# Kernel optimization log

Hardware: AMD Instinct MI355X
Metric: run time of the kernel (lower is better)

The kernel has to match this reference:

```python
import jax, jax.numpy as jnp
import numpy as np

CTX = 2048
N_EMBD = 1024
HEAD = 128

def setup_inputs() -> dict:
    key = jax.random.key(0)
    kx, kq, kk, kv = jax.random.split(key, 4)
    s = 1.0 / np.sqrt(N_EMBD)
    return {
        "x": jax.random.normal(kx, (4, CTX, N_EMBD), dtype=jnp.float32),
        "Wq": jax.random.normal(kq, (N_EMBD, HEAD), dtype=jnp.float32) * s,
        "Wk": jax.random.normal(kk, (N_EMBD, HEAD), dtype=jnp.float32) * s,
        "Wv": jax.random.normal(kv, (N_EMBD, HEAD), dtype=jnp.float32) * s,
    }

def reference(x, Wq, Wk, Wv):
    B, T, C = x.shape
    q = jnp.einsum('btc,ch->bth', x, Wq)
    k = jnp.einsum('btc,ch->bth', x, Wk)
    v = jnp.einsum('btc,ch->bth', x, Wv)
    scale = 1.0 / jnp.sqrt(jnp.asarray(k.shape[-1], dtype=x.dtype))
    wei = jnp.einsum('bth,bsh->bts', q, k) * scale  # [B,T,T]
    causal = jnp.tril(jnp.ones((T, T), dtype=bool))
    wei = jnp.where(causal, wei, jnp.asarray(-jnp.inf, dtype=wei.dtype))
    wei = jax.nn.softmax(wei, axis=-1)
    out = jnp.einsum('bts,bsh->bth', wei, v)
    return out
```

## Files before the change

kernel.cpp:

```cpp
#include <hip/hip_runtime.h>

#define BATCH 4
#define CTX   2048
#define EMB   1024
#define HEAD  128

typedef __attribute__((ext_vector_type(8))) short bf16x8;
typedef __attribute__((ext_vector_type(4))) float f32x4;
typedef const __attribute__((address_space(1))) unsigned int* gas_t;
typedef __attribute__((address_space(3))) unsigned int* las_t;

#define FINF (__builtin_inff())
__device__ inline float fexp2(float x) { return __builtin_amdgcn_exp2f(x); }

__device__ inline void cp16(const void* g, void* l) {
    __builtin_amdgcn_global_load_lds((gas_t)g, (las_t)l, 16, 0, 0);
}

__device__ inline unsigned short f2bf(float f) {
    union { float f; unsigned u; } v; v.f = f;
    unsigned r = v.u + 0x7fffu + ((v.u >> 16) & 1u);
    return (unsigned short)(r >> 16);
}
__device__ inline unsigned pk2(float a, float b) {
    return (unsigned)f2bf(a) | ((unsigned)f2bf(b) << 16);
}
__device__ inline float bf2f(unsigned u16) {
    union { unsigned u; float f; } v; v.u = u16 << 16; return v.f;
}

__global__ __launch_bounds__(256)
void transpose_w_kernel(const float* __restrict__ Wq, const float* __restrict__ Wk,
                        const float* __restrict__ Wv, unsigned short* __restrict__ Wt) {
    const int k0 = blockIdx.x * 64;
    const int h0 = blockIdx.y * 64;
    const int w  = blockIdx.z;
    const float* W = (w == 0) ? Wq : (w == 1) ? Wk : Wv;
    __shared__ float Ts[64][65];
    const int tid = threadIdx.x;
    #pragma unroll
    for (int it = 0; it < 4; ++it) {
        const int kk = (tid >> 4) + it * 16;
        const int c4 = (tid & 15) * 4;
        const float4 f = *(const float4*)&W[(size_t)(k0 + kk) * HEAD + h0 + c4];
        Ts[kk][c4 + 0] = f.x; Ts[kk][c4 + 1] = f.y;
        Ts[kk][c4 + 2] = f.z; Ts[kk][c4 + 3] = f.w;
    }
    __syncthreads();
    const int hr  = tid >> 2;
    const int kc0 = (tid & 3) * 16;
    union { unsigned short s[16]; uint4 q[2]; } tmp;
    #pragma unroll
    for (int i = 0; i < 16; ++i) tmp.s[i] = f2bf(Ts[kc0 + i][hr]);
    unsigned short* dst = &Wt[(size_t)w * HEAD * EMB + (size_t)(h0 + hr) * EMB + k0 + kc0];
    ((uint4*)dst)[0] = tmp.q[0];
    ((uint4*)dst)[1] = tmp.q[1];
}

__global__ __launch_bounds__(128, 3)
void proj_kernel(const float* __restrict__ x, const unsigned short* __restrict__ Wt,
                 unsigned short* __restrict__ qb, unsigned short* __restrict__ kb,
                 unsigned short* __restrict__ vt) {
    __shared__ __align__(16) char smem[24576];
    char* Ab = smem;
    char* Bb = smem + 8192;

    const int wsel = blockIdx.y;
    const int tid  = threadIdx.x;
    const int wv   = tid >> 6;
    const int lane = tid & 63;
    const int p = lane >> 4, c = lane & 15;
    const int m0 = blockIdx.x * 32;
    const unsigned short* Wp = Wt + (size_t)wsel * HEAD * EMB;

    const int u7  = c & 7;
    const int u2c = (c ^ (c >> 2)) & 3;

    auto stage = [&](int bi, int ks) {
        #pragma unroll
        for (int i = 0; i < 2; ++i) {
            const int f = i * 128 + tid;
            const int r = f >> 3, s = f & 7, q = s ^ (r & 7);
            cp16(&x[(size_t)(m0 + r) * EMB + ks * 32 + q * 4],
                 Ab + bi * 4096 + i * 2048 + wv * 1024);
        }
        #pragma unroll
        for (int i = 0; i < 4; ++i) {
            const int f = i * 128 + tid;
            const int h = f >> 2, s = f & 3, q = s ^ ((h ^ (h >> 2)) & 3);
            cp16(&Wp[(size_t)h * EMB + ks * 32 + q * 8],
                 Bb + bi * 8192 + i * 2048 + wv * 1024);
        }
    };
    auto xfrag = [&](const char* Ac, int r) {
        const float4 a0 = *(const float4*)(Ac + r * 128 + (((2 * p)     ^ u7) * 16));
        const float4 a1 = *(const float4*)(Ac + r * 128 + (((2 * p + 1) ^ u7) * 16));
        union { unsigned u[4]; bf16x8 v; } xf;
        xf.u[0] = pk2(a0.x, a0.y); xf.u[1] = pk2(a0.z, a0.w);
        xf.u[2] = pk2(a1.x, a1.y); xf.u[3] = pk2(a1.z, a1.w);
        return xf.v;
    };

    if (wsel < 2) {
        f32x4 acc[8];
        #pragma unroll
        for (int i = 0; i < 8; ++i) acc[i] = (f32x4){0.f, 0.f, 0.f, 0.f};
        stage(0, 0);
        for (int ks = 0; ks < 32; ++ks) {
            const int cur = ks & 1;
            __syncthreads();
            if (ks + 1 < 32) stage(cur ^ 1, ks + 1);
            const bf16x8 xv = xfrag(Ab + cur * 4096, wv * 16 + c);
            const char* Bc = Bb + cur * 8192;
            #pragma unroll
            for (int nt = 0; nt < 8; ++nt) {
                const int h = nt * 16 + c;
                const bf16x8 wf = *(const bf16x8*)(Bc + h * 64 + ((p ^ u2c) * 16));
                acc[nt] = __builtin_amdgcn_mfma_f32_16x16x32_bf16(xv, wf, acc[nt], 0, 0, 0);
            }
        }
        unsigned short* outp = (wsel == 0) ? qb : kb;
        #pragma unroll
        for (int rr = 0; rr < 4; ++rr) {
            unsigned short* orow = outp + (size_t)(m0 + wv * 16 + p * 4 + rr) * HEAD + c;
            #pragma unroll
            for (int nt = 0; nt < 8; ++nt)
                orow[nt * 16] = f2bf(acc[nt][rr]);
        }
    } else {
        f32x4 acc[4][2];
        #pragma unroll
        for (int i = 0; i < 4; ++i)
            #pragma unroll
            for (int j = 0; j < 2; ++j) acc[i][j] = (f32x4){0.f, 0.f, 0.f, 0.f};
        stage(0, 0);
        for (int ks = 0; ks < 32; ++ks) {
            const int cur = ks & 1;
            __syncthreads();
            if (ks + 1 < 32) stage(cur ^ 1, ks + 1);
            const char* Ac = Ab + cur * 4096;
            const char* Bc = Bb + cur * 8192;
            bf16x8 xv[2];
            #pragma unroll
            for (int n2 = 0; n2 < 2; ++n2) xv[n2] = xfrag(Ac, n2 * 16 + c);
            #pragma unroll
            for (int mt = 0; mt < 4; ++mt) {
                const int h = wv * 64 + mt * 16 + c;
                const bf16x8 wf = *(const bf16x8*)(Bc + h * 64 + ((p ^ u2c) * 16));
                #pragma unroll
                for (int n2 = 0; n2 < 2; ++n2)
                    acc[mt][n2] = __builtin_amdgcn_mfma_f32_16x16x32_bf16(wf, xv[n2], acc[mt][n2], 0, 0, 0);
            }
        }
        const int bidx = m0 >> 11;
        const int tl   = m0 & (CTX - 1);
        unsigned short* vbp = vt + (size_t)bidx * HEAD * CTX;
        #pragma unroll
        for (int mt = 0; mt < 4; ++mt)
            #pragma unroll
            for (int rr = 0; rr < 4; ++rr) {
                const int h = wv * 64 + mt * 16 + p * 4 + rr;
                #pragma unroll
                for (int n2 = 0; n2 < 2; ++n2)
                    vbp[(size_t)h * CTX + tl + n2 * 16 + c] = f2bf(acc[mt][n2][rr]);
            }
    }
}

__global__ __launch_bounds__(256, 2)
void attn_split_kernel(const unsigned short* __restrict__ qb,
                       const unsigned short* __restrict__ kb,
                       const unsigned short* __restrict__ vt,
                       unsigned short* __restrict__ pO,
                       float* __restrict__ pM, float* __restrict__ pL) {
    __shared__ __align__(16) char smem[65536];
    char* Kb = smem;
    char* Vb = smem + 32768;

    const int g = blockIdx.x;
    const int b = blockIdx.y;
    int T, ch;
    if (g < 8)       { T = g;                ch = 0; }
    else if (g < 24) { T = 8  + ((g - 8) >> 1);  ch = (g - 8) & 1; }
    else if (g < 48) { T = 16 + (g - 24) / 3;    ch = (g - 24) % 3; }
    else             { T = 24 + ((g - 48) >> 2); ch = (g - 48) & 3; }
    const int nch    = (T >> 3) + 1;
    const int kstart = ch * 512;
    const int kend   = min(kstart + 512, 64 * (T + 1));
    const int nsteps = (kend - kstart) >> 6;
    const bool lastchunk = (ch == nch - 1);

    const int tid  = threadIdx.x;
    const int wv   = tid >> 6;
    const int lane = tid & 63;
    const int p = lane >> 4, c = lane & 15;
    const int t0 = T * 64;
    const int qg = t0 + wv * 16 + c;
    const int u7 = c & 7;

    const unsigned short* kbat = kb + (size_t)b * CTX * HEAD;
    const unsigned short* vbat = vt + (size_t)b * HEAD * CTX;

    bf16x8 qf[4];
    #pragma unroll
    for (int ks = 0; ks < 4; ++ks)
        qf[ks] = *(const bf16x8*)&qb[((size_t)b * CTX + t0 + wv * 16 + c) * HEAD + ks * 32 + p * 8];

    f32x4 o[8];
    #pragma unroll
    for (int i = 0; i < 8; ++i) o[i] = (f32x4){0.f, 0.f, 0.f, 0.f};
    float m = -FINF, l = 0.f;

    const int  slA = 32 * (p & 1) + c;
    const int  slB = slA + 16;
    const bool thi = (p >> 1) != 0;
    const float scale2 = 0.08838834764831845f * 1.44269504088896340f;

    auto stage = [&](int bi, int js) {
        const unsigned short* kg = kbat + (size_t)(kstart + js * 64) * HEAD;
        #pragma unroll
        for (int i = 0; i < 4; ++i) {
            const int f = i * 256 + tid;
            const int r = f >> 4, s = f & 15, q = s ^ (r & 7);
            cp16(kg + (size_t)r * HEAD + q * 8, Kb + bi * 16384 + (f >> 6) * 1024);
        }
        const unsigned short* vg = vbat + kstart + js * 64;
        #pragma unroll
        for (int i = 0; i < 4; ++i) {
            const int f = i * 256 + tid;
            const int r = f >> 3, s = f & 7, q = s ^ (r & 7);
            cp16(vg + (size_t)r * CTX + q * 8, Vb + bi * 16384 + (f >> 6) * 1024);
        }
    };

    stage(0, 0);
    for (int js = 0; js < nsteps; ++js) {
        const int cur = js & 1;
        __builtin_amdgcn_s_waitcnt(0);
        __syncthreads();

        bf16x8 kfr[4][4];
        #pragma unroll
        for (int nt = 0; nt < 4; ++nt) {
            const char* rp = Kb + cur * 16384 + (nt * 16 + c) * 256;
            #pragma unroll
            for (int ks = 0; ks < 4; ++ks)
                kfr[nt][ks] = *(const bf16x8*)(rp + (((ks * 4 + p) ^ u7) * 16));
        }
        if (js + 1 < nsteps) stage(cur ^ 1, js + 1);

        f32x4 st[4];
        #pragma unroll
        for (int nt = 0; nt < 4; ++nt) st[nt] = (f32x4){0.f, 0.f, 0.f, 0.f};
        #pragma unroll
        for (int ks = 0; ks < 4; ++ks)
            #pragma unroll
            for (int nt = 0; nt < 4; ++nt)
                st[nt] = __builtin_amdgcn_mfma_f32_16x16x32_bf16(kfr[nt][ks], qf[ks], st[nt], 0, 0, 0);

        bf16x8 vfr[2][8];
        #pragma unroll
        for (int mt = 0; mt < 8; ++mt) {
            const char* rp = Vb + cur * 16384 + (mt * 16 + c) * 128;
            #pragma unroll
            for (int ch2 = 0; ch2 < 2; ++ch2)
                vfr[ch2][mt] = *(const bf16x8*)(rp + (((ch2 * 4 + p) ^ u7) * 16));
        }

        float s[4][4];
        float lm = -FINF;
        if (lastchunk && js == nsteps - 1) {
            #pragma unroll
            for (int nt = 0; nt < 4; ++nt)
                #pragma unroll
                for (int r = 0; r < 4; ++r) {
                    const int kv = kstart + js * 64 + nt * 16 + p * 4 + r;
                    float v = st[nt][r] * scale2;
                    v = (kv <= qg) ? v : -FINF;
                    s[nt][r] = v;
                    lm = fmaxf(lm, v);
                }
        } else {
            #pragma unroll
            for (int nt = 0; nt < 4; ++nt)
                #pragma unroll
                for (int r = 0; r < 4; ++r) {
                    const float v = st[nt][r] * scale2;
                    s[nt][r] = v;
                    lm = fmaxf(lm, v);
                }
        }
        lm = fmaxf(lm, __shfl_xor(lm, 16, 64));
        lm = fmaxf(lm, __shfl_xor(lm, 32, 64));
        const float m_new = fmaxf(m, lm);
        const float alpha = fexp2(m - m_new);
        float ls = 0.f;
        #pragma unroll
        for (int nt = 0; nt < 4; ++nt)
            #pragma unroll
            for (int r = 0; r < 4; ++r) {
                const float pv = fexp2(s[nt][r] - m_new);
                s[nt][r] = pv;
                ls += pv;
            }
        ls += __shfl_xor(ls, 16, 64);
        ls += __shfl_xor(ls, 32, 64);
        l = l * alpha + ls;
        m = m_new;
        #pragma unroll
        for (int i = 0; i < 8; ++i) {
            o[i][0] *= alpha; o[i][1] *= alpha;
            o[i][2] *= alpha; o[i][3] *= alpha;
        }
        #pragma unroll
        for (int ch2 = 0; ch2 < 2; ++ch2) {
            const unsigned pa0 = pk2(s[2*ch2][0],     s[2*ch2][1]);
            const unsigned pb0 = pk2(s[2*ch2][2],     s[2*ch2][3]);
            const unsigned pa1 = pk2(s[2*ch2 + 1][0], s[2*ch2 + 1][1]);
            const unsigned pb1 = pk2(s[2*ch2 + 1][2], s[2*ch2 + 1][3]);
            const unsigned u0a = __shfl((int)pa0, slA, 64), u0b = __shfl((int)pa1, slA, 64);
            const unsigned u1a = __shfl((int)pb0, slA, 64), u1b = __shfl((int)pb1, slA, 64);
            const unsigned u2a = __shfl((int)pa0, slB, 64), u2b = __shfl((int)pa1, slB, 64);
            const unsigned u3a = __shfl((int)pb0, slB, 64), u3b = __shfl((int)pb1, slB, 64);
            union { unsigned u[4]; bf16x8 v; } pf;
            pf.u[0] = thi ? u0b : u0a;
            pf.u[1] = thi ? u1b : u1a;
            pf.u[2] = thi ? u2b : u2a;
            pf.u[3] = thi ? u3b : u3a;
            #pragma unroll
            for (int mt = 0; mt < 8; ++mt)
                o[mt] = __builtin_amdgcn_mfma_f32_16x16x32_bf16(vfr[ch2][mt], pf.v, o[mt], 0, 0, 0);
        }
    }

    const size_t pbase = (size_t)(b * 32 + T) * 4 + ch;
    unsigned short* po = pO + pbase * (64 * 128) + (wv * 16 + c) * 128;
    #pragma unroll
    for (int mt = 0; mt < 8; ++mt) {
        union { unsigned short sh[4]; uint2 u; } t;
        #pragma unroll
        for (int r = 0; r < 4; ++r) t.sh[r] = f2bf(o[mt][r]);
        *(uint2*)&po[mt * 16 + p * 4] = t.u;
    }
    if (p == 0) {
        pM[pbase * 64 + wv * 16 + c] = m;
        pL[pbase * 64 + wv * 16 + c] = l;
    }
}

__global__ __launch_bounds__(256)
void attn_merge_kernel(const unsigned short* __restrict__ pO,
                       const float* __restrict__ pM, const float* __restrict__ pL,
                       float* __restrict__ out) {
    const int T = blockIdx.x, b = blockIdx.y;
    const int nch = (T >> 3) + 1;
    const int tid = threadIdx.x;
    const int r   = tid >> 2;
    const int c0  = (tid & 3) * 32;
    const size_t base = (size_t)(b * 32 + T) * 4;

    float mv[4], lv[4];
    float M = -FINF;
    #pragma unroll
    for (int i = 0; i < 4; ++i) {
        if (i < nch) { mv[i] = pM[(base + i) * 64 + r]; lv[i] = pL[(base + i) * 64 + r]; }
        else         { mv[i] = -FINF;                   lv[i] = 0.f; }
        M = fmaxf(M, mv[i]);
    }
    float w[4], L = 0.f;
    #pragma unroll
    for (int i = 0; i < 4; ++i) { w[i] = fexp2(mv[i] - M); L += w[i] * lv[i]; }
    const float inv = 1.f / L;

    float acc[32];
    #pragma unroll
    for (int j = 0; j < 32; ++j) acc[j] = 0.f;
    #pragma unroll
    for (int i = 0; i < 4; ++i) {
        if (i < nch) {
            const unsigned* s32 = (const unsigned*)(pO + (base + i) * (64 * 128) + r * 128 + c0);
            const float wi = w[i];
            #pragma unroll
            for (int jw = 0; jw < 16; ++jw) {
                const unsigned u = s32[jw];
                acc[2 * jw]     += wi * bf2f(u & 0xffffu);
                acc[2 * jw + 1] += wi * bf2f(u >> 16);
            }
        }
    }
    float* orow = out + ((size_t)b * CTX + T * 64 + r) * HEAD + c0;
    #pragma unroll
    for (int j4 = 0; j4 < 8; ++j4) {
        float4 ov = make_float4(acc[4*j4] * inv, acc[4*j4+1] * inv,
                                acc[4*j4+2] * inv, acc[4*j4+3] * inv);
        *(float4*)&orow[4 * j4] = ov;
    }
}

__global__ __launch_bounds__(64, 1)
void attn_kernel(const unsigned short* __restrict__ qb,
                 const unsigned short* __restrict__ kb,
                 const unsigned short* __restrict__ vt,
                 float* __restrict__ out) {
    __shared__ __align__(16) char smem[65536];
    char* Kb = smem;
    char* Vb = smem + 32768;
    const int bx   = blockIdx.x;
    const int b    = bx & 3;
    const int tile = 127 - (bx >> 2);
    const int lane = threadIdx.x;
    const int p = lane >> 4, c = lane & 15;
    const int t0 = tile * 16;
    const int qg = t0 + c;
    const int u7 = c & 7;
    const unsigned short* kbat = kb + (size_t)b * CTX * HEAD;
    const unsigned short* vbat = vt + (size_t)b * HEAD * CTX;
    bf16x8 qf[4];
    #pragma unroll
    for (int ks = 0; ks < 4; ++ks)
        qf[ks] = *(const bf16x8*)&qb[((size_t)b * CTX + t0 + c) * HEAD + ks * 32 + p * 8];
    f32x4 o[8];
    #pragma unroll
    for (int i = 0; i < 8; ++i) o[i] = (f32x4){0.f, 0.f, 0.f, 0.f};
    float m = -FINF, l = 0.f;
    const int  slA = 32 * (p & 1) + c;
    const int  slB = slA + 16;
    const bool thi = (p >> 1) != 0;
    const int  nsteps = (tile + 4) >> 2;
    const float scale2 = 0.08838834764831845f * 1.44269504088896340f;
    auto stage = [&](int bi, int js) {
        const unsigned short* kg = kbat + (size_t)(js * 64) * HEAD;
        #pragma unroll
        for (int i = 0; i < 16; ++i) {
            const int f = i * 64 + lane;
            const int r = f >> 4, s = f & 15, q = s ^ (r & 7);
            cp16(kg + (size_t)r * HEAD + q * 8, Kb + bi * 16384 + i * 1024);
        }
        #pragma unroll
        for (int i = 0; i < 16; ++i) {
            const int f = i * 64 + lane;
            const int r = f >> 3, s = f & 7, q = s ^ (r & 7);
            cp16(vbat + (size_t)r * CTX + js * 64 + q * 8, Vb + bi * 16384 + i * 1024);
        }
    };
    stage(0, 0);
    for (int js = 0; js < nsteps; ++js) {
        const int cur = js & 1;
        __builtin_amdgcn_s_waitcnt(0);
        bf16x8 kfr[4][4], vfr[2][8];
        #pragma unroll
        for (int nt = 0; nt < 4; ++nt) {
            const char* rp = Kb + cur * 16384 + (nt * 16 + c) * 256;
            #pragma unroll
            for (int ks = 0; ks < 4; ++ks)
                kfr[nt][ks] = *(const bf16x8*)(rp + (((ks * 4 + p) ^ u7) * 16));
        }
        #pragma unroll
        for (int mt = 0; mt < 8; ++mt) {
            const char* rp = Vb + cur * 16384 + (mt * 16 + c) * 128;
            #pragma unroll
            for (int ch = 0; ch < 2; ++ch)
                vfr[ch][mt] = *(const bf16x8*)(rp + (((ch * 4 + p) ^ u7) * 16));
        }
        if (js + 1 < nsteps) stage(cur ^ 1, js + 1);
        const int c0 = js * 64;
        f32x4 st[4];
        #pragma unroll
        for (int nt = 0; nt < 4; ++nt) st[nt] = (f32x4){0.f, 0.f, 0.f, 0.f};
        #pragma unroll
        for (int ks = 0; ks < 4; ++ks)
            #pragma unroll
            for (int nt = 0; nt < 4; ++nt)
                st[nt] = __builtin_amdgcn_mfma_f32_16x16x32_bf16(kfr[nt][ks], qf[ks], st[nt], 0, 0, 0);
        float s[4][4];
        float lm = -FINF;
        if (js == nsteps - 1) {
            #pragma unroll
            for (int nt = 0; nt < 4; ++nt)
                #pragma unroll
                for (int r = 0; r < 4; ++r) {
                    const int kv = c0 + nt * 16 + p * 4 + r;
                    float v = st[nt][r] * scale2;
                    v = (kv <= qg) ? v : -FINF;
                    s[nt][r] = v;
                    lm = fmaxf(lm, v);
                }
        } else {
            #pragma unroll
            for (int nt = 0; nt < 4; ++nt)
                #pragma unroll
                for (int r = 0; r < 4; ++r) {
                    const float v = st[nt][r] * scale2;
                    s[nt][r] = v;
                    lm = fmaxf(lm, v);
                }
        }
        lm = fmaxf(lm, __shfl_xor(lm, 16, 64));
        lm = fmaxf(lm, __shfl_xor(lm, 32, 64));
        const float m_new = fmaxf(m, lm);
        const float alpha = fexp2(m - m_new);
        float ls = 0.f;
        #pragma unroll
        for (int nt = 0; nt < 4; ++nt)
            #pragma unroll
            for (int r = 0; r < 4; ++r) {
                const float pv = fexp2(s[nt][r] - m_new);
                s[nt][r] = pv;
                ls += pv;
            }
        ls += __shfl_xor(ls, 16, 64);
        ls += __shfl_xor(ls, 32, 64);
        l = l * alpha + ls;
        m = m_new;
        #pragma unroll
        for (int i = 0; i < 8; ++i) {
            o[i][0] *= alpha; o[i][1] *= alpha;
            o[i][2] *= alpha; o[i][3] *= alpha;
        }
        #pragma unroll
        for (int ch = 0; ch < 2; ++ch) {
            const unsigned pa0 = pk2(s[2*ch][0],     s[2*ch][1]);
            const unsigned pb0 = pk2(s[2*ch][2],     s[2*ch][3]);
            const unsigned pa1 = pk2(s[2*ch + 1][0], s[2*ch + 1][1]);
            const unsigned pb1 = pk2(s[2*ch + 1][2], s[2*ch + 1][3]);
            const unsigned u0a = __shfl((int)pa0, slA, 64), u0b = __shfl((int)pa1, slA, 64);
            const unsigned u1a = __shfl((int)pb0, slA, 64), u1b = __shfl((int)pb1, slA, 64);
            const unsigned u2a = __shfl((int)pa0, slB, 64), u2b = __shfl((int)pa1, slB, 64);
            const unsigned u3a = __shfl((int)pb0, slB, 64), u3b = __shfl((int)pb1, slB, 64);
            union { unsigned u[4]; bf16x8 v; } pf;
            pf.u[0] = thi ? u0b : u0a;
            pf.u[1] = thi ? u1b : u1a;
            pf.u[2] = thi ? u2b : u2a;
            pf.u[3] = thi ? u3b : u3a;
            #pragma unroll
            for (int mt = 0; mt < 8; ++mt)
                o[mt] = __builtin_amdgcn_mfma_f32_16x16x32_bf16(vfr[ch][mt], pf.v, o[mt], 0, 0, 0);
        }
    }
    const float linv = 1.f / l;
    float* orow = out + ((size_t)b * CTX + t0 + c) * HEAD;
    #pragma unroll
    for (int mt = 0; mt < 8; ++mt) {
        float4 ov = make_float4(o[mt][0] * linv, o[mt][1] * linv,
                                o[mt][2] * linv, o[mt][3] * linv);
        *(float4*)&orow[mt * 16 + p * 4] = ov;
    }
}

extern "C" void kernel_launch(void* const* d_in, const int* in_sizes, int n_in,
                              void* d_out, int out_size, void* d_ws, size_t ws_size,
                              hipStream_t stream) {
    const float* x  = (const float*)d_in[0];
    const float* Wq = (const float*)d_in[1];
    const float* Wk = (const float*)d_in[2];
    const float* Wv = (const float*)d_in[3];
    float* out = (float*)d_out;

    unsigned short* Wt = (unsigned short*)d_ws;
    unsigned short* qb = Wt + (size_t)3 * HEAD * EMB;
    unsigned short* kb = qb + (size_t)BATCH * CTX * HEAD;
    unsigned short* vt = kb + (size_t)BATCH * CTX * HEAD;
    unsigned short* pO = vt + (size_t)BATCH * CTX * HEAD;
    float* pM = (float*)(pO + (size_t)BATCH * 32 * 4 * 64 * 128);
    float* pL = pM + (size_t)BATCH * 32 * 4 * 64;

    const size_t need = (size_t)((char*)(pL + BATCH * 32 * 4 * 64) - (char*)d_ws);

    transpose_w_kernel<<<dim3(16, 2, 3), 256, 0, stream>>>(Wq, Wk, Wv, Wt);
    proj_kernel<<<dim3((BATCH * CTX) / 32, 3), 128, 0, stream>>>(x, Wt, qb, kb, vt);
    if (ws_size >= need) {
        attn_split_kernel<<<dim3(80, 4), 256, 0, stream>>>(qb, kb, vt, pO, pM, pL);
        attn_merge_kernel<<<dim3(32, 4), 256, 0, stream>>>(pO, pM, pL, out);
    } else {
        attn_kernel<<<BATCH * (CTX / 16), 64, 0, stream>>>(qb, kb, vt, out);
    }
}
```

Baseline: 126.0 us.

## Halve attention KV chunk size and give each wave two query subtiles

The split-KV attention kernel now uses 256-key chunks instead of 512, which raises the grid from 80 to 144 blocks per batch. Blocks shrink to 128 threads, with each wave handling two 16-row query subtiles so K/V fragments loaded from LDS are reused across both. The aim is better load balance and more parallelism across CUs for the causal workload, plus more reuse of each K/V fragment. In exchange it doubles per-wave register state, drops the occupancy hint to 1, and makes the merge kernel combine up to 8 partials with more partial-output traffic.

Result: slower. 131.5 us (+4.4%).

```diff
diff --git a/kernel.cpp b/kernel.cpp
--- a/kernel.cpp
+++ b/kernel.cpp
@@ -167,7 +167,7 @@
     }
 }
 
-__global__ __launch_bounds__(256, 2)
+__global__ __launch_bounds__(128, 1)
 void attn_split_kernel(const unsigned short* __restrict__ qb,
                        const unsigned short* __restrict__ kb,
                        const unsigned short* __restrict__ vt,
@@ -179,37 +179,41 @@
 
     const int g = blockIdx.x;
     const int b = blockIdx.y;
-    int T, ch;
-    if (g < 8)       { T = g;                ch = 0; }
-    else if (g < 24) { T = 8  + ((g - 8) >> 1);  ch = (g - 8) & 1; }
-    else if (g < 48) { T = 16 + (g - 24) / 3;    ch = (g - 24) % 3; }
-    else             { T = 24 + ((g - 48) >> 2); ch = (g - 48) & 3; }
-    const int nch    = (T >> 3) + 1;
-    const int kstart = ch * 512;
-    const int kend   = min(kstart + 512, 64 * (T + 1));
-    const int nsteps = (kend - kstart) >> 6;
-    const bool lastchunk = (ch == nch - 1);
+    int a = 0;
+    while (a < 7 && g >= 2 * (a + 1) * (a + 2)) ++a;
+    const int rem = g - 2 * a * (a + 1);
+    const int T   = 4 * a + rem / (a + 1);
+    const int ch  = rem % (a + 1);
+    const bool lastchunk = (ch == a);
+    const int kstart = ch * 256;
+    const int nsteps = lastchunk ? ((T & 3) + 1) : 4;
 
     const int tid  = threadIdx.x;
     const int wv   = tid >> 6;
     const int lane = tid & 63;
     const int p = lane >> 4, c = lane & 15;
     const int t0 = T * 64;
-    const int qg = t0 + wv * 16 + c;
     const int u7 = c & 7;
+    int qg[2];
+    qg[0] = t0 + wv * 32 + c;
+    qg[1] = qg[0] + 16;
 
     const unsigned short* kbat = kb + (size_t)b * CTX * HEAD;
     const unsigned short* vbat = vt + (size_t)b * HEAD * CTX;
 
-    bf16x8 qf[4];
-    #pragma unroll
-    for (int ks = 0; ks < 4; ++ks)
-        qf[ks] = *(const bf16x8*)&qb[((size_t)b * CTX + t0 + wv * 16 + c) * HEAD + ks * 32 + p * 8];
-
-    f32x4 o[8];
-    #pragma unroll
-    for (int i = 0; i < 8; ++i) o[i] = (f32x4){0.f, 0.f, 0.f, 0.f};
-    float m = -FINF, l = 0.f;
+    bf16x8 qf[2][4];
+    #pragma unroll
+    for (int qs = 0; qs < 2; ++qs)
+        #pragma unroll
+        for (int ks = 0; ks < 4; ++ks)
+            qf[qs][ks] = *(const bf16x8*)&qb[((size_t)b * CTX + t0 + wv * 32 + qs * 16 + c) * HEAD + ks * 32 + p * 8];
+
+    f32x4 o[2][8];
+    #pragma unroll
+    for (int qs = 0; qs < 2; ++qs)
+        #pragma unroll
+        for (int i = 0; i < 8; ++i) o[qs][i] = (f32x4){0.f, 0.f, 0.f, 0.f};
+    float m2[2] = {-FINF, -FINF}, l2[2] = {0.f, 0.f};
 
     const int  slA = 32 * (p & 1) + c;
     const int  slB = slA + 16;
@@ -219,15 +223,15 @@
     auto stage = [&](int bi, int js) {
         const unsigned short* kg = kbat + (size_t)(kstart + js * 64) * HEAD;
         #pragma unroll
-        for (int i = 0; i < 4; ++i) {
-            const int f = i * 256 + tid;
+        for (int i = 0; i < 8; ++i) {
+            const int f = i * 128 + tid;
             const int r = f >> 4, s = f & 15, q = s ^ (r & 7);
             cp16(kg + (size_t)r * HEAD + q * 8, Kb + bi * 16384 + (f >> 6) * 1024);
         }
         const unsigned short* vg = vbat + kstart + js * 64;
         #pragma unroll
-        for (int i = 0; i < 4; ++i) {
-            const int f = i * 256 + tid;
+        for (int i = 0; i < 8; ++i) {
+            const int f = i * 128 + tid;
             const int r = f >> 3, s = f & 7, q = s ^ (r & 7);
             cp16(vg + (size_t)r * CTX + q * 8, Vb + bi * 16384 + (f >> 6) * 1024);
         }
@@ -249,102 +253,114 @@
         }
         if (js + 1 < nsteps) stage(cur ^ 1, js + 1);
 
-        f32x4 st[4];
-        #pragma unroll
-        for (int nt = 0; nt < 4; ++nt) st[nt] = (f32x4){0.f, 0.f, 0.f, 0.f};
+        f32x4 st[2][4];
+        #pragma unroll
+        for (int qs = 0; qs < 2; ++qs)
+            #pragma unroll
+            for (int nt = 0; nt < 4; ++nt) st[qs][nt] = (f32x4){0.f, 0.f, 0.f, 0.f};
         #pragma unroll
         for (int ks = 0; ks < 4; ++ks)
             #pragma unroll
-            for (int nt = 0; nt < 4; ++nt)
-                st[nt] = __builtin_amdgcn_mfma_f32_16x16x32_bf16(kfr[nt][ks], qf[ks], st[nt], 0, 0, 0);
+            for (int nt = 0; nt < 4; ++nt) {
+                st[0][nt] = __builtin_amdgcn_mfma_f32_16x16x32_bf16(kfr[nt][ks], qf[0][ks], st[0][nt], 0, 0, 0);
+                st[1][nt] = __builtin_amdgcn_mfma_f32_16x16x32_bf16(kfr[nt][ks], qf[1][ks], st[1][nt], 0, 0, 0);
+            }
 
         bf16x8 vfr[2][8];
         #pragma unroll
         for (int mt = 0; mt < 8; ++mt) {
             const char* rp = Vb + cur * 16384 + (mt * 16 + c) * 128;
             #pragma unroll
-            for (int ch2 = 0; ch2 < 2; ++ch2)
-                vfr[ch2][mt] = *(const bf16x8*)(rp + (((ch2 * 4 + p) ^ u7) * 16));
-        }
-
-        float s[4][4];
-        float lm = -FINF;
-        if (lastchunk && js == nsteps - 1) {
+            for (int c2 = 0; c2 < 2; ++c2)
+                vfr[c2][mt] = *(const bf16x8*)(rp + (((c2 * 4 + p) ^ u7) * 16));
+        }
+
+        const bool domask = lastchunk && (js == nsteps - 1);
+        float s[2][4][4];
+        #pragma unroll
+        for (int qs = 0; qs < 2; ++qs) {
+            float lm = -FINF;
+            if (domask) {
+                #pragma unroll
+                for (int nt = 0; nt < 4; ++nt)
+                    #pragma unroll
+                    for (int r = 0; r < 4; ++r) {
+                        const int kv = kstart + js * 64 + nt * 16 + p * 4 + r;
+                        float v = st[qs][nt][r] * scale2;
+                        v = (kv <= qg[qs]) ? v : -FINF;
+                        s[qs][nt][r] = v;
+                        lm = fmaxf(lm, v);
+                    }
+            } else {
+                #pragma unroll
+                for (int nt = 0; nt < 4; ++nt)
+                    #pragma unroll
+                    for (int r = 0; r < 4; ++r) {
+                        const float v = st[qs][nt][r] * scale2;
+                        s[qs][nt][r] = v;
+                        lm = fmaxf(lm, v);
+                    }
+            }
+            lm = fmaxf(lm, __shfl_xor(lm, 16, 64));
+            lm = fmaxf(lm, __shfl_xor(lm, 32, 64));
+            const float m_new = fmaxf(m2[qs], lm);
+            const float alpha = fexp2(m2[qs] - m_new);
+            float ls = 0.f;
             #pragma unroll
             for (int nt = 0; nt < 4; ++nt)
                 #pragma unroll
                 for (int r = 0; r < 4; ++r) {
-                    const int kv = kstart + js * 64 + nt * 16 + p * 4 + r;
-                    float v = st[nt][r] * scale2;
-                    v = (kv <= qg) ? v : -FINF;
-                    s[nt][r] = v;
-                    lm = fmaxf(lm, v);
+                    const float pv = fexp2(s[qs][nt][r] - m_new);
+                    s[qs][nt][r] = pv;
+                    ls += pv;
                 }
-        } else {
-            #pragma unroll
-            for (int nt = 0; nt < 4; ++nt)
-                #pragma unroll
-                for (int r = 0; r < 4; ++r) {
-                    const float v = st[nt][r] * scale2;
-                    s[nt][r] = v;
-                    lm = fmaxf(lm, v);
-                }
-        }
-        lm = fmaxf(lm, __shfl_xor(lm, 16, 64));
-        lm = fmaxf(lm, __shfl_xor(lm, 32, 64));
-        const float m_new = fmaxf(m, lm);
-        const float alpha = fexp2(m - m_new);
-        float ls = 0.f;
-        #pragma unroll
-        for (int nt = 0; nt < 4; ++nt)
-            #pragma unroll
-            for (int r = 0; r < 4; ++r) {
-                const float pv = fexp2(s[nt][r] - m_new);
-                s[nt][r] = pv;
-                ls += pv;
-            }
-        ls += __shfl_xor(ls, 16, 64);
-        ls += __shfl_xor(ls, 32, 64);
-        l = l * alpha + ls;
-        m = m_new;
-        #pragma unroll
-        for (int i = 0; i < 8; ++i) {
-            o[i][0] *= alpha; o[i][1] *= alpha;
-            o[i][2] *= alpha; o[i][3] *= alpha;
-        }
-        #pragma unroll
-        for (int ch2 = 0; ch2 < 2; ++ch2) {
-            const unsigned pa0 = pk2(s[2*ch2][0],     s[2*ch2][1]);
-            const unsigned pb0 = pk2(s[2*ch2][2],     s[2*ch2][3]);
-            const unsigned pa1 = pk2(s[2*ch2 + 1][0], s[2*ch2 + 1][1]);
-            const unsigned pb1 = pk2(s[2*ch2 + 1][2], s[2*ch2 + 1][3]);
-            const unsigned u0a = __shfl((int)pa0, slA, 64), u0b = __shfl((int)pa1, slA, 64);
-            const unsigned u1a = __shfl((int)pb0, slA, 64), u1b = __shfl((int)pb1, slA, 64);
-            const unsigned u2a = __shfl((int)pa0, slB, 64), u2b = __shfl((int)pa1, slB, 64);
-            const unsigned u3a = __shfl((int)pb0, slB, 64), u3b = __shfl((int)pb1, slB, 64);
-            union { unsigned u[4]; bf16x8 v; } pf;
-            pf.u[0] = thi ? u0b : u0a;
-            pf.u[1] = thi ? u1b : u1a;
-            pf.u[2] = thi ? u2b : u2a;
-            pf.u[3] = thi ? u3b : u3a;
-            #pragma unroll
-            for (int mt = 0; mt < 8; ++mt)
-                o[mt] = __builtin_amdgcn_mfma_f32_16x16x32_bf16(vfr[ch2][mt], pf.v, o[mt], 0, 0, 0);
-        }
-    }
-
-    const size_t pbase = (size_t)(b * 32 + T) * 4 + ch;
-    unsigned short* po = pO + pbase * (64 * 128) + (wv * 16 + c) * 128;
-    #pragma unroll
-    for (int mt = 0; mt < 8; ++mt) {
-        union { unsigned short sh[4]; uint2 u; } t;
-        #pragma unroll
-        for (int r = 0; r < 4; ++r) t.sh[r] = f2bf(o[mt][r]);
-        *(uint2*)&po[mt * 16 + p * 4] = t.u;
-    }
-    if (p == 0) {
-        pM[pbase * 64 + wv * 16 + c] = m;
-        pL[pbase * 64 + wv * 16 + c] = l;
+            ls += __shfl_xor(ls, 16, 64);
+            ls += __shfl_xor(ls, 32, 64);
+            l2[qs] = l2[qs] * alpha + ls;
+            m2[qs] = m_new;
+            #pragma unroll
+            for (int i = 0; i < 8; ++i) {
+                o[qs][i][0] *= alpha; o[qs][i][1] *= alpha;
+                o[qs][i][2] *= alpha; o[qs][i][3] *= alpha;
+            }
+            #pragma unroll
+            for (int c2 = 0; c2 < 2; ++c2) {
+                const unsigned pa0 = pk2(s[qs][2*c2][0],     s[qs][2*c2][1]);
+                const unsigned pb0 = pk2(s[qs][2*c2][2],     s[qs][2*c2][3]);
+                const unsigned pa1 = pk2(s[qs][2*c2 + 1][0], s[qs][2*c2 + 1][1]);
+                const unsigned pb1 = pk2(s[qs][2*c2 + 1][2], s[qs][2*c2 + 1][3]);
+                const unsigned u0a = __shfl((int)pa0, slA, 64), u0b = __shfl((int)pa1, slA, 64);
+                const unsigned u1a = __shfl((int)pb0, slA, 64), u1b = __shfl((int)pb1, slA, 64);
+                const unsigned u2a = __shfl((int)pa0, slB, 64), u2b = __shfl((int)pa1, slB, 64);
+                const unsigned u3a = __shfl((int)pb0, slB, 64), u3b = __shfl((int)pb1, slB, 64);
+                union { unsigned u[4]; bf16x8 v; } pf;
+                pf.u[0] = thi ? u0b : u0a;
+                pf.u[1] = thi ? u1b : u1a;
+                pf.u[2] = thi ? u2b : u2a;
+                pf.u[3] = thi ? u3b : u3a;
+                #pragma unroll
+                for (int mt = 0; mt < 8; ++mt)
+                    o[qs][mt] = __builtin_amdgcn_mfma_f32_16x16x32_bf16(vfr[c2][mt], pf.v, o[qs][mt], 0, 0, 0);
+            }
+        }
+    }
+
+    const size_t pbase = (size_t)(b * 32 + T) * 8 + ch;
+    unsigned short* po = pO + pbase * (64 * 128);
+    #pragma unroll
+    for (int qs = 0; qs < 2; ++qs) {
+        unsigned short* prow = po + (wv * 32 + qs * 16 + c) * 128;
+        #pragma unroll
+        for (int mt = 0; mt < 8; ++mt) {
+            union { unsigned short sh[4]; uint2 u; } t;
+            #pragma unroll
+            for (int r = 0; r < 4; ++r) t.sh[r] = f2bf(o[qs][mt][r]);
+            *(uint2*)&prow[mt * 16 + p * 4] = t.u;
+        }
+        if (p == 0) {
+            pM[pbase * 64 + wv * 32 + qs * 16 + c] = m2[qs];
+            pL[pbase * 64 + wv * 32 + qs * 16 + c] = l2[qs];
+        }
     }
 }
 
@@ -353,30 +369,30 @@
                        const float* __restrict__ pM, const float* __restrict__ pL,
                        float* __restrict__ out) {
     const int T = blockIdx.x, b = blockIdx.y;
-    const int nch = (T >> 3) + 1;
+    const int nch = (T >> 2) + 1;
     const int tid = threadIdx.x;
     const int r   = tid >> 2;
     const int c0  = (tid & 3) * 32;
-    const size_t base = (size_t)(b * 32 + T) * 4;
-
-    float mv[4], lv[4];
+    const size_t base = (size_t)(b * 32 + T) * 8;
+
+    float mv[8], lv[8];
     float M = -FINF;
     #pragma unroll
-    for (int i = 0; i < 4; ++i) {
+    for (int i = 0; i < 8; ++i) {
         if (i < nch) { mv[i] = pM[(base + i) * 64 + r]; lv[i] = pL[(base + i) * 64 + r]; }
         else         { mv[i] = -FINF;                   lv[i] = 0.f; }
         M = fmaxf(M, mv[i]);
     }
-    float w[4], L = 0.f;
-    #pragma unroll
-    for (int i = 0; i < 4; ++i) { w[i] = fexp2(mv[i] - M); L += w[i] * lv[i]; }
+    float w[8], L = 0.f;
+    #pragma unroll
+    for (int i = 0; i < 8; ++i) { w[i] = fexp2(mv[i] - M); L += w[i] * lv[i]; }
     const float inv = 1.f / L;
 
     float acc[32];
     #pragma unroll
     for (int j = 0; j < 32; ++j) acc[j] = 0.f;
     #pragma unroll
-    for (int i = 0; i < 4; ++i) {
+    for (int i = 0; i < 8; ++i) {
         if (i < nch) {
             const unsigned* s32 = (const unsigned*)(pO + (base + i) * (64 * 128) + r * 128 + c0);
             const float wi = w[i];
@@ -561,15 +577,15 @@
     unsigned short* kb = qb + (size_t)BATCH * CTX * HEAD;
     unsigned short* vt = kb + (size_t)BATCH * CTX * HEAD;
     unsigned short* pO = vt + (size_t)BATCH * CTX * HEAD;
-    float* pM = (float*)(pO + (size_t)BATCH * 32 * 4 * 64 * 128);
-    float* pL = pM + (size_t)BATCH * 32 * 4 * 64;
-
-    const size_t need = (size_t)((char*)(pL + BATCH * 32 * 4 * 64) - (char*)d_ws);
+    float* pM = (float*)(pO + (size_t)BATCH * 32 * 8 * 64 * 128);
+    float* pL = pM + (size_t)BATCH * 32 * 8 * 64;
+
+    const size_t need = (size_t)((char*)(pL + BATCH * 32 * 8 * 64) - (char*)d_ws);
 
     transpose_w_kernel<<<dim3(16, 2, 3), 256, 0, stream>>>(Wq, Wk, Wv, Wt);
     proj_kernel<<<dim3((BATCH * CTX) / 32, 3), 128, 0, stream>>>(x, Wt, qb, kb, vt);
     if (ws_size >= need) {
-        attn_split_kernel<<<dim3(80, 4), 256, 0, stream>>>(qb, kb, vt, pO, pM, pL);
+        attn_split_kernel<<<dim3(144, 4), 128, 0, stream>>>(qb, kb, vt, pO, pM, pL);
         attn_merge_kernel<<<dim3(32, 4), 256, 0, stream>>>(pO, pM, pL, out);
     } else {
         attn_kernel<<<BATCH * (CTX / 16), 64, 0, stream>>>(qb, kb, vt, out);
```

## Run projection kernel as single wave per block, replacing barriers with waitcnt

Applied to the files above, without the earlier changes.

The projection kernel now uses one 64-lane wavefront per block instead of two, so the wave computes the full 32x128 output tile itself. Block-wide __syncthreads is replaced with s_waitcnt(0), and all LDS fragments are read into registers before the next stage's async copies are issued. The goal is to remove barrier overhead and overlap the global-to-LDS copies with the MFMA work. In exchange, each wave holds twice as many accumulators, launch bounds drop to 64 threads per block with a minimum of 1 block, and register pressure and occupancy may change.

Result: faster. 123.1 us (median of 2 runs) (-2.2%).

```diff
diff --git a/kernel.cpp b/kernel.cpp
--- a/kernel.cpp
+++ b/kernel.cpp
@@ -57,7 +57,7 @@
     ((uint4*)dst)[1] = tmp.q[1];
 }
 
-__global__ __launch_bounds__(128, 3)
+__global__ __launch_bounds__(64, 1)
 void proj_kernel(const float* __restrict__ x, const unsigned short* __restrict__ Wt,
                  unsigned short* __restrict__ qb, unsigned short* __restrict__ kb,
                  unsigned short* __restrict__ vt) {
@@ -66,9 +66,7 @@
     char* Bb = smem + 8192;
 
     const int wsel = blockIdx.y;
-    const int tid  = threadIdx.x;
-    const int wv   = tid >> 6;
-    const int lane = tid & 63;
+    const int lane = threadIdx.x;
     const int p = lane >> 4, c = lane & 15;
     const int m0 = blockIdx.x * 32;
     const unsigned short* Wp = Wt + (size_t)wsel * HEAD * EMB;
@@ -78,18 +76,18 @@
 
     auto stage = [&](int bi, int ks) {
         #pragma unroll
-        for (int i = 0; i < 2; ++i) {
-            const int f = i * 128 + tid;
+        for (int i = 0; i < 4; ++i) {
+            const int f = i * 64 + lane;
             const int r = f >> 3, s = f & 7, q = s ^ (r & 7);
             cp16(&x[(size_t)(m0 + r) * EMB + ks * 32 + q * 4],
-                 Ab + bi * 4096 + i * 2048 + wv * 1024);
-        }
-        #pragma unroll
-        for (int i = 0; i < 4; ++i) {
-            const int f = i * 128 + tid;
+                 Ab + bi * 4096 + i * 1024);
+        }
+        #pragma unroll
+        for (int i = 0; i < 8; ++i) {
+            const int f = i * 64 + lane;
             const int h = f >> 2, s = f & 3, q = s ^ ((h ^ (h >> 2)) & 3);
             cp16(&Wp[(size_t)h * EMB + ks * 32 + q * 8],
-                 Bb + bi * 8192 + i * 2048 + wv * 1024);
+                 Bb + bi * 8192 + i * 1024);
         }
     };
     auto xfrag = [&](const char* Ac, int r) {
@@ -101,68 +99,63 @@
         return xf.v;
     };
 
+    f32x4 acc[2][8];
+    #pragma unroll
+    for (int i = 0; i < 2; ++i)
+        #pragma unroll
+        for (int j = 0; j < 8; ++j) acc[i][j] = (f32x4){0.f, 0.f, 0.f, 0.f};
+
+    stage(0, 0);
+    for (int ks = 0; ks < 32; ++ks) {
+        const int cur = ks & 1;
+        __builtin_amdgcn_s_waitcnt(0);
+        const char* Ac = Ab + cur * 4096;
+        const char* Bc = Bb + cur * 8192;
+        bf16x8 xv[2], wf[8];
+        #pragma unroll
+        for (int mi = 0; mi < 2; ++mi) xv[mi] = xfrag(Ac, mi * 16 + c);
+        #pragma unroll
+        for (int nt = 0; nt < 8; ++nt)
+            wf[nt] = *(const bf16x8*)(Bc + (nt * 16 + c) * 64 + ((p ^ u2c) * 16));
+        if (ks + 1 < 32) stage(cur ^ 1, ks + 1);
+        if (wsel < 2) {
+            #pragma unroll
+            for (int mi = 0; mi < 2; ++mi)
+                #pragma unroll
+                for (int nt = 0; nt < 8; ++nt)
+                    acc[mi][nt] = __builtin_amdgcn_mfma_f32_16x16x32_bf16(xv[mi], wf[nt], acc[mi][nt], 0, 0, 0);
+        } else {
+            #pragma unroll
+            for (int n2 = 0; n2 < 2; ++n2)
+                #pragma unroll
+                for (int mt = 0; mt < 8; ++mt)
+                    acc[n2][mt] = __builtin_amdgcn_mfma_f32_16x16x32_bf16(wf[mt], xv[n2], acc[n2][mt], 0, 0, 0);
+        }
+    }
+
     if (wsel < 2) {
-        f32x4 acc[8];
-        #pragma unroll
-        for (int i = 0; i < 8; ++i) acc[i] = (f32x4){0.f, 0.f, 0.f, 0.f};
-        stage(0, 0);
-        for (int ks = 0; ks < 32; ++ks) {
-            const int cur = ks & 1;
-            __syncthreads();
-            if (ks + 1 < 32) stage(cur ^ 1, ks + 1);
-            const bf16x8 xv = xfrag(Ab + cur * 4096, wv * 16 + c);
-            const char* Bc = Bb + cur * 8192;
-            #pragma unroll
-            for (int nt = 0; nt < 8; ++nt) {
-                const int h = nt * 16 + c;
-                const bf16x8 wf = *(const bf16x8*)(Bc + h * 64 + ((p ^ u2c) * 16));
-                acc[nt] = __builtin_amdgcn_mfma_f32_16x16x32_bf16(xv, wf, acc[nt], 0, 0, 0);
+        unsigned short* outp = (wsel == 0) ? qb : kb;
+        #pragma unroll
+        for (int mi = 0; mi < 2; ++mi)
+            #pragma unroll
+            for (int rr = 0; rr < 4; ++rr) {
+                unsigned short* orow = outp + (size_t)(m0 + mi * 16 + p * 4 + rr) * HEAD + c;
+                #pragma unroll
+                for (int nt = 0; nt < 8; ++nt)
+                    orow[nt * 16] = f2bf(acc[mi][nt][rr]);
             }
-        }
-        unsigned short* outp = (wsel == 0) ? qb : kb;
-        #pragma unroll
-        for (int rr = 0; rr < 4; ++rr) {
-            unsigned short* orow = outp + (size_t)(m0 + wv * 16 + p * 4 + rr) * HEAD + c;
-            #pragma unroll
-            for (int nt = 0; nt < 8; ++nt)
-                orow[nt * 16] = f2bf(acc[nt][rr]);
-        }
     } else {
-        f32x4 acc[4][2];
-        #pragma unroll
-        for (int i = 0; i < 4; ++i)
-            #pragma unroll
-            for (int j = 0; j < 2; ++j) acc[i][j] = (f32x4){0.f, 0.f, 0.f, 0.f};
-        stage(0, 0);
-        for (int ks = 0; ks < 32; ++ks) {
-            const int cur = ks & 1;
-            __syncthreads();
-            if (ks + 1 < 32) stage(cur ^ 1, ks + 1);
-            const char* Ac = Ab + cur * 4096;
-            const char* Bc = Bb + cur * 8192;
-            bf16x8 xv[2];
-            #pragma unroll
-            for (int n2 = 0; n2 < 2; ++n2) xv[n2] = xfrag(Ac, n2 * 16 + c);
-            #pragma unroll
-            for (int mt = 0; mt < 4; ++mt) {
-                const int h = wv * 64 + mt * 16 + c;
-                const bf16x8 wf = *(const bf16x8*)(Bc + h * 64 + ((p ^ u2c) * 16));
-                #pragma unroll
-                for (int n2 = 0; n2 < 2; ++n2)
-                    acc[mt][n2] = __builtin_amdgcn_mfma_f32_16x16x32_bf16(wf, xv[n2], acc[mt][n2], 0, 0, 0);
-            }
-        }
         const int bidx = m0 >> 11;
         const int tl   = m0 & (CTX - 1);
         unsigned short* vbp = vt + (size_t)bidx * HEAD * CTX;
         #pragma unroll
-        for (int mt = 0; mt < 4; ++mt)
+        for (int mt = 0; mt < 8; ++mt)
             #pragma unroll
             for (int rr = 0; rr < 4; ++rr) {
-                const int h = wv * 64 + mt * 16 + p * 4 + rr;
+                const int h = mt * 16 + p * 4 + rr;
                 #pragma unroll
                 for (int n2 = 0; n2 < 2; ++n2)
-                    vbp[(size_t)h * CTX + tl + n2 * 16 + c] = f2bf(acc[mt][n2][rr]);
+                    vbp[(size_t)h * CTX + tl + n2 * 16 + c] = f2bf(acc[n2][mt][rr]);
             }
     }
 }
@@ -567,7 +560,7 @@
     const size_t need = (size_t)((char*)(pL + BATCH * 32 * 4 * 64) - (char*)d_ws);
 
     transpose_w_kernel<<<dim3(16, 2, 3), 256, 0, stream>>>(Wq, Wk, Wv, Wt);
-    proj_kernel<<<dim3((BATCH * CTX) / 32, 3), 128, 0, stream>>>(x, Wt, qb, kb, vt);
+    proj_kernel<<<dim3((BATCH * CTX) / 32, 3), 64, 0, stream>>>(x, Wt, qb, kb, vt);
     if (ws_size >= need) {
         attn_split_kernel<<<dim3(80, 4), 256, 0, stream>>>(qb, kb, vt, pO, pM, pL);
         attn_merge_kernel<<<dim3(32, 4), 256, 0, stream>>>(pO, pM, pL, out);
```
